# Optimization experiments

Measured on AMD Instinct MI355X. Metric: run time of the kernel, lower is better.

## Reference

```python
import jax, jax.numpy as jnp
import numpy as np

B, T, D, H = 512, 2048, 256, 256  # batch, seq_len, input_size, hidden_size


def _uniform(key, shape, fan_in):
    b = 1.0 / np.sqrt(fan_in)
    return jax.random.uniform(key, shape, minval=-b, maxval=b, dtype=jnp.float32)


def setup_inputs() -> dict:
    key = jax.random.key(0)
    ks = jax.random.split(key, 12)
    return {
        "input_tensor": jax.random.normal(ks[0], (B, T, D), dtype=jnp.float32),
        # fc_i: Linear(D, D)
        "Wi": _uniform(ks[1], (D, D), D), "bi": _uniform(ks[2], (D,), D),
        # fc_h: Linear(H, H)
        "Wh": _uniform(ks[3], (H, H), H), "bh": _uniform(ks[4], (H,), H),
        # fc_a: Linear(D, D)
        "Wa": _uniform(ks[5], (D, D), D), "ba": _uniform(ks[6], (D,), D),
        # LSTM(input_size=D, hidden_size=H), gates ordered [i, f, g, o]
        "W_ih": _uniform(ks[7], (4 * H, D), H), "b_ih": _uniform(ks[8], (4 * H,), H),
        "W_hh": _uniform(ks[9], (4 * H, H), H), "b_hh": _uniform(ks[10], (4 * H,), H),
    }


def reference(input_tensor, Wi, bi, Wh, bh, Wa, ba, W_ih, W_hh, b_ih, b_hh):
    x = input_tensor                      # (B, T, D)
    Bb = x.shape[0]
    Hh = Wh.shape[0]
    h0 = jnp.zeros((Bb, Hh), x.dtype)
    c0 = jnp.zeros((Bb, Hh), x.dtype)

    # Per-timestep FC attention; hidden state never updates in the loop,
    # so it vectorizes exactly over T.
    input_o = jnp.einsum('btd,ed->bte', x, Wi) + bi          # (B, T, D)
    hidden_o = h0 @ Wh.T + bh                                # (B, H) == (B, D)
    pre = input_o + hidden_o[:, None, :]                     # (B, T, D)
    attn = jax.nn.sigmoid(jnp.einsum('btd,ed->bte', pre, Wa) + ba)
    attention_output = jnp.sum(attn * x, axis=1)             # (B, D)

    # LSTM over a length-1 sequence (single cell step), PyTorch gate order i,f,g,o
    gates = attention_output @ W_ih.T + b_ih + h0 @ W_hh.T + b_hh
    i, f, g, o = jnp.split(gates, 4, axis=-1)
    i = jax.nn.sigmoid(i); f = jax.nn.sigmoid(f)
    g = jnp.tanh(g); o = jax.nn.sigmoid(o)
    c = f * c0 + i * g
    h = o * jnp.tanh(c)

    lstm_output = h[None]                                    # (1, B, H)
    return (lstm_output, h[None], c[None])
```

## Files before the change

### kernel.cpp

```cpp
#include <hip/hip_runtime.h>
#include <hip/hip_bf16.h>

typedef _Float16 f16x8 __attribute__((ext_vector_type(8)));
typedef float    f32x4 __attribute__((ext_vector_type(4)));

#define B_SZ 512
#define T_SZ 2048
#define D_SZ 256
#define TCHUNK 64
#define NCHUNK (T_SZ / TCHUNK)

__global__ __launch_bounds__(256) void prep_kernel(
    const float* __restrict__ Wa, const float* __restrict__ Wi,
    const float* __restrict__ bi, const float* __restrict__ bh,
    const float* __restrict__ ba,
    _Float16* __restrict__ Weff, float* __restrict__ beff)
{
    int e = blockIdx.x;
    int d = threadIdx.x;
    float acc = 0.f;
    #pragma unroll 4
    for (int k = 0; k < 256; ++k)
        acc = fmaf(Wa[e*256 + k], Wi[k*256 + d], acc);
    Weff[e*256 + d] = (_Float16)acc;

    __shared__ float red[256];
    red[d] = Wa[e*256 + d] * (bi[d] + bh[d]);
    __syncthreads();
    if (d == 0) {
        float s = ba[e];
        for (int k = 0; k < 256; ++k) s += red[k];
        beff[e] = s;
    }
}

__global__ __launch_bounds__(512) void attn_kernel(
    const float* __restrict__ x,
    const _Float16* __restrict__ Weff,
    const float* __restrict__ beff,
    float* __restrict__ ao)
{
    const int b    = blockIdx.x;
    const int tid  = threadIdx.x;
    const int wave = tid >> 6;
    const int lane = tid & 63;
    const int l15  = lane & 15;
    const int lq   = lane >> 4;

    __shared__ _Float16 xs[TCHUNK * 256];

    f16x8 bfrag[2][8];
    #pragma unroll
    for (int ct = 0; ct < 2; ++ct) {
        int col = wave*32 + ct*16 + l15;
        #pragma unroll
        for (int ks = 0; ks < 8; ++ks) {
            int k0 = ks*32 + lq*8;
            bfrag[ct][ks] = *reinterpret_cast<const f16x8*>(&Weff[col*256 + k0]);
        }
    }
    float bcol[2];
    bcol[0] = beff[wave*32 + l15];
    bcol[1] = beff[wave*32 + 16 + l15];

    const float* xb = x + (size_t)b * T_SZ * D_SZ;

    const int srow = tid >> 5;
    const int scol = (tid & 31) * 8;

    f32x4 regA[4], regB[4];

    {
        const float* src = xb;
        #pragma unroll
        for (int i = 0; i < 4; ++i) {
            const float* p = src + (size_t)(i*16 + srow) * 256 + scol;
            regA[i] = *reinterpret_cast<const f32x4*>(p);
            regB[i] = *reinterpret_cast<const f32x4*>(p + 4);
        }
    }

    float ao_acc0 = 0.f, ao_acc1 = 0.f;

    for (int c = 0; c < NCHUNK; ++c) {
        __syncthreads();
        #pragma unroll
        for (int i = 0; i < 4; ++i) {
            int row = i*16 + srow;
            f16x8 h;
            h[0] = (_Float16)regA[i][0]; h[1] = (_Float16)regA[i][1];
            h[2] = (_Float16)regA[i][2]; h[3] = (_Float16)regA[i][3];
            h[4] = (_Float16)regB[i][0]; h[5] = (_Float16)regB[i][1];
            h[6] = (_Float16)regB[i][2]; h[7] = (_Float16)regB[i][3];
            int byte = (row*512 + scol*2) ^ ((row & 7) << 4);
            *reinterpret_cast<f16x8*>(reinterpret_cast<char*>(xs) + byte) = h;
        }
        __syncthreads();

        if (c + 1 < NCHUNK) {
            const float* src = xb + (size_t)(c + 1) * (TCHUNK * D_SZ);
            #pragma unroll
            for (int i = 0; i < 4; ++i) {
                const float* p = src + (size_t)(i*16 + srow) * 256 + scol;
                regA[i] = *reinterpret_cast<const f32x4*>(p);
                regB[i] = *reinterpret_cast<const f32x4*>(p + 4);
            }
        }

        #pragma unroll
        for (int rt = 0; rt < 4; ++rt) {
            f16x8 afrag[8];
            #pragma unroll
            for (int ks = 0; ks < 8; ++ks) {
                int row = rt*16 + l15;
                int kk  = ks*32 + lq*8;
                int byte = (row*512 + kk*2) ^ ((row & 7) << 4);
                afrag[ks] = *reinterpret_cast<const f16x8*>(
                    reinterpret_cast<const char*>(xs) + byte);
            }
            #pragma unroll
            for (int ct = 0; ct < 2; ++ct) {
                f32x4 acc = {0.f, 0.f, 0.f, 0.f};
                #pragma unroll
                for (int ks = 0; ks < 8; ++ks)
                    acc = __builtin_amdgcn_mfma_f32_16x16x32_f16(
                        afrag[ks], bfrag[ct][ks], acc, 0, 0, 0);
                float bia = bcol[ct];
                int colb = (wave*32 + ct*16 + l15) * 2;
                #pragma unroll
                for (int r = 0; r < 4; ++r) {
                    int row = rt*16 + lq*4 + r;
                    float s = acc[r] + bia;
                    float attn = __builtin_amdgcn_rcpf(1.f + __expf(-s));
                    int byte = (row*512 + colb) ^ ((row & 7) << 4);
                    float xv = (float)*reinterpret_cast<const _Float16*>(
                        reinterpret_cast<const char*>(xs) + byte);
                    if (ct == 0) ao_acc0 = fmaf(attn, xv, ao_acc0);
                    else         ao_acc1 = fmaf(attn, xv, ao_acc1);
                }
            }
        }
    }

    {
        float v = ao_acc0;
        v += __shfl_xor(v, 16, 64);
        v += __shfl_xor(v, 32, 64);
        if (lq == 0) ao[b*256 + wave*32 + l15] = v;
        float w = ao_acc1;
        w += __shfl_xor(w, 16, 64);
        w += __shfl_xor(w, 32, 64);
        if (lq == 0) ao[b*256 + wave*32 + 16 + l15] = w;
    }
}

__global__ __launch_bounds__(256) void lstm_kernel(
    const float* __restrict__ ao,
    const float* __restrict__ Wih,
    const float* __restrict__ bih,
    const float* __restrict__ bhh,
    float* __restrict__ out)
{
    int b = blockIdx.x;
    int j = threadIdx.x;
    __shared__ float a[256];
    a[j] = ao[b*256 + j];
    __syncthreads();

    float gi = bih[j]       + bhh[j];
    float gg = bih[512 + j] + bhh[512 + j];
    float go = bih[768 + j] + bhh[768 + j];
    const float* wi = Wih + (size_t)j * 256;
    const float* wg = Wih + (size_t)(512 + j) * 256;
    const float* wo = Wih + (size_t)(768 + j) * 256;
    #pragma unroll 4
    for (int k = 0; k < 256; k += 4) {
        f32x4 w1 = *reinterpret_cast<const f32x4*>(wi + k);
        f32x4 w2 = *reinterpret_cast<const f32x4*>(wg + k);
        f32x4 w3 = *reinterpret_cast<const f32x4*>(wo + k);
        #pragma unroll
        for (int q = 0; q < 4; ++q) {
            float av = a[k + q];
            gi = fmaf(w1[q], av, gi);
            gg = fmaf(w2[q], av, gg);
            go = fmaf(w3[q], av, go);
        }
    }
    float ig = 1.f / (1.f + __expf(-gi));
    float g  = tanhf(gg);
    float og = 1.f / (1.f + __expf(-go));
    float cc = ig * g;
    float hh = og * tanhf(cc);
    out[          b*256 + j] = hh;
    out[131072 +  b*256 + j] = hh;
    out[262144 +  b*256 + j] = cc;
}

extern "C" void kernel_launch(void* const* d_in, const int* in_sizes, int n_in,
                              void* d_out, int out_size, void* d_ws, size_t ws_size,
                              hipStream_t stream) {
    const float* x    = (const float*)d_in[0];
    const float* Wi   = (const float*)d_in[1];
    const float* bi   = (const float*)d_in[2];
    const float* bh   = (const float*)d_in[4];
    const float* Wa   = (const float*)d_in[5];
    const float* ba   = (const float*)d_in[6];
    const float* W_ih = (const float*)d_in[7];
    const float* b_ih = (const float*)d_in[8];
    const float* b_hh = (const float*)d_in[10];

    char* ws = (char*)d_ws;
    _Float16* Weff = (_Float16*)ws;
    float*    beff = (float*)(ws + 128*1024);
    float*    ao   = (float*)(ws + 132*1024);

    prep_kernel<<<256, 256, 0, stream>>>(Wa, Wi, bi, bh, ba, Weff, beff);
    attn_kernel<<<B_SZ, 512, 0, stream>>>(x, Weff, beff, ao);
    lstm_kernel<<<B_SZ, 256, 0, stream>>>(ao, W_ih, b_ih, b_hh, (float*)d_out);
}
```

Before: 308.8 us.

## Double-buffer x chunks via direct global-to-LDS loads in fp32

The attention kernel now streams x straight into a double-buffered fp32 LDS tile using global_load_lds, in place of loading into registers and converting to fp16 before the shared store. Conversion to fp16 moves to the point where MFMA A-fragments are read. The chunk shrinks to 32 rows so two fp32 buffers fit, and waitcnt/barrier fencing overlaps the next chunk's load with compute. The prep kernel also gets split accumulators and a wave-shuffle bias reduction. This trades more LDS bandwidth and per-fragment conversion work for fewer register staging copies and better load/compute overlap.

After: 420.8 us. 1.36x slower.

```diff
diff --git a/kernel.cpp b/kernel.cpp
--- a/kernel.cpp
+++ b/kernel.cpp
@@ -7,7 +7,7 @@
 #define B_SZ 512
 #define T_SZ 2048
 #define D_SZ 256
-#define TCHUNK 64
+#define TCHUNK 32
 #define NCHUNK (T_SZ / TCHUNK)
 
 __global__ __launch_bounds__(256) void prep_kernel(
@@ -18,23 +18,30 @@
 {
     int e = blockIdx.x;
     int d = threadIdx.x;
-    float acc = 0.f;
+    float a0 = 0.f, a1 = 0.f, a2 = 0.f, a3 = 0.f;
     #pragma unroll 4
-    for (int k = 0; k < 256; ++k)
-        acc = fmaf(Wa[e*256 + k], Wi[k*256 + d], acc);
-    Weff[e*256 + d] = (_Float16)acc;
-
-    __shared__ float red[256];
-    red[d] = Wa[e*256 + d] * (bi[d] + bh[d]);
+    for (int k = 0; k < 256; k += 4) {
+        a0 = fmaf(Wa[e*256 + k    ], Wi[(k    )*256 + d], a0);
+        a1 = fmaf(Wa[e*256 + k + 1], Wi[(k + 1)*256 + d], a1);
+        a2 = fmaf(Wa[e*256 + k + 2], Wi[(k + 2)*256 + d], a2);
+        a3 = fmaf(Wa[e*256 + k + 3], Wi[(k + 3)*256 + d], a3);
+    }
+    Weff[e*256 + d] = (_Float16)((a0 + a1) + (a2 + a3));
+
+    __shared__ float red[4];
+    float s = Wa[e*256 + d] * (bi[d] + bh[d]);
+    s += __shfl_down(s, 32, 64);
+    s += __shfl_down(s, 16, 64);
+    s += __shfl_down(s,  8, 64);
+    s += __shfl_down(s,  4, 64);
+    s += __shfl_down(s,  2, 64);
+    s += __shfl_down(s,  1, 64);
+    if ((d & 63) == 0) red[d >> 6] = s;
     __syncthreads();
-    if (d == 0) {
-        float s = ba[e];
-        for (int k = 0; k < 256; ++k) s += red[k];
-        beff[e] = s;
-    }
-}
-
-__global__ __launch_bounds__(512) void attn_kernel(
+    if (d == 0) beff[e] = ba[e] + ((red[0] + red[1]) + (red[2] + red[3]));
+}
+
+__global__ __launch_bounds__(512, 4) void attn_kernel(
     const float* __restrict__ x,
     const _Float16* __restrict__ Weff,
     const float* __restrict__ beff,
@@ -47,7 +54,7 @@
     const int l15  = lane & 15;
     const int lq   = lane >> 4;
 
-    __shared__ _Float16 xs[TCHUNK * 256];
+    __shared__ float xs[2][TCHUNK * 256];
 
     f16x8 bfrag[2][8];
     #pragma unroll
@@ -59,99 +66,97 @@
             bfrag[ct][ks] = *reinterpret_cast<const f16x8*>(&Weff[col*256 + k0]);
         }
     }
-    float bcol[2];
-    bcol[0] = beff[wave*32 + l15];
-    bcol[1] = beff[wave*32 + 16 + l15];
+    float bcol0 = beff[wave*32 + l15];
+    float bcol1 = beff[wave*32 + 16 + l15];
 
     const float* xb = x + (size_t)b * T_SZ * D_SZ;
 
-    const int srow = tid >> 5;
-    const int scol = (tid & 31) * 8;
-
-    f32x4 regA[4], regB[4];
-
-    {
-        const float* src = xb;
+    #define STAGE(dstbuf, c)                                                          \
+        {                                                                             \
+            _Pragma("unroll")                                                         \
+            for (int i = 0; i < 4; ++i) {                                             \
+                int rw = wave*4 + i;                                                  \
+                int gcol = (lane*16) ^ ((rw & 7) << 4);                               \
+                const char* srcp = (const char*)(xb + (size_t)((c)*TCHUNK + rw)*256) + gcol; \
+                char* dstp = (char*)(&xs[dstbuf][0]) + rw*1024;                       \
+                __builtin_amdgcn_global_load_lds(                                     \
+                    (const __attribute__((address_space(1))) void*)srcp,              \
+                    (__attribute__((address_space(3))) void*)dstp, 16, 0, 0);         \
+            }                                                                         \
+        }
+
+    float ao_acc0 = 0.f, ao_acc1 = 0.f;
+
+    STAGE(0, 0);
+    int cur = 0;
+
+    for (int c = 0; c < NCHUNK; ++c) {
+        if (c + 1 < NCHUNK) {
+            STAGE(cur ^ 1, c + 1);
+            asm volatile("s_waitcnt vmcnt(4)" ::: "memory");
+        } else {
+            asm volatile("s_waitcnt vmcnt(0)" ::: "memory");
+        }
+        __builtin_amdgcn_s_barrier();
+
+        const char* buf = (const char*)(&xs[cur][0]);
+
         #pragma unroll
-        for (int i = 0; i < 4; ++i) {
-            const float* p = src + (size_t)(i*16 + srow) * 256 + scol;
-            regA[i] = *reinterpret_cast<const f32x4*>(p);
-            regB[i] = *reinterpret_cast<const f32x4*>(p + 4);
-        }
-    }
-
-    float ao_acc0 = 0.f, ao_acc1 = 0.f;
-
-    for (int c = 0; c < NCHUNK; ++c) {
-        __syncthreads();
-        #pragma unroll
-        for (int i = 0; i < 4; ++i) {
-            int row = i*16 + srow;
-            f16x8 h;
-            h[0] = (_Float16)regA[i][0]; h[1] = (_Float16)regA[i][1];
-            h[2] = (_Float16)regA[i][2]; h[3] = (_Float16)regA[i][3];
-            h[4] = (_Float16)regB[i][0]; h[5] = (_Float16)regB[i][1];
-            h[6] = (_Float16)regB[i][2]; h[7] = (_Float16)regB[i][3];
-            int byte = (row*512 + scol*2) ^ ((row & 7) << 4);
-            *reinterpret_cast<f16x8*>(reinterpret_cast<char*>(xs) + byte) = h;
-        }
-        __syncthreads();
-
-        if (c + 1 < NCHUNK) {
-            const float* src = xb + (size_t)(c + 1) * (TCHUNK * D_SZ);
-            #pragma unroll
-            for (int i = 0; i < 4; ++i) {
-                const float* p = src + (size_t)(i*16 + srow) * 256 + scol;
-                regA[i] = *reinterpret_cast<const f32x4*>(p);
-                regB[i] = *reinterpret_cast<const f32x4*>(p + 4);
-            }
-        }
-
-        #pragma unroll
-        for (int rt = 0; rt < 4; ++rt) {
-            f16x8 afrag[8];
+        for (int rt = 0; rt < 2; ++rt) {
+            const int arow = rt*16 + l15;
+            const int aswz = (arow & 7) << 4;
+            const int abase = arow*1024;
+            f32x4 acc0 = {0.f, 0.f, 0.f, 0.f};
+            f32x4 acc1 = {0.f, 0.f, 0.f, 0.f};
             #pragma unroll
             for (int ks = 0; ks < 8; ++ks) {
-                int row = rt*16 + l15;
-                int kk  = ks*32 + lq*8;
-                int byte = (row*512 + kk*2) ^ ((row & 7) << 4);
-                afrag[ks] = *reinterpret_cast<const f16x8*>(
-                    reinterpret_cast<const char*>(xs) + byte);
+                int cb0 = ks*128 + lq*32;
+                f32x4 lo = *reinterpret_cast<const f32x4*>(buf + abase + ((cb0     ) ^ aswz));
+                f32x4 hi = *reinterpret_cast<const f32x4*>(buf + abase + ((cb0 + 16) ^ aswz));
+                f16x8 a;
+                a[0] = (_Float16)lo[0]; a[1] = (_Float16)lo[1];
+                a[2] = (_Float16)lo[2]; a[3] = (_Float16)lo[3];
+                a[4] = (_Float16)hi[0]; a[5] = (_Float16)hi[1];
+                a[6] = (_Float16)hi[2]; a[7] = (_Float16)hi[3];
+                acc0 = __builtin_amdgcn_mfma_f32_16x16x32_f16(a, bfrag[0][ks], acc0, 0, 0, 0);
+                acc1 = __builtin_amdgcn_mfma_f32_16x16x32_f16(a, bfrag[1][ks], acc1, 0, 0, 0);
             }
             #pragma unroll
-            for (int ct = 0; ct < 2; ++ct) {
-                f32x4 acc = {0.f, 0.f, 0.f, 0.f};
-                #pragma unroll
-                for (int ks = 0; ks < 8; ++ks)
-                    acc = __builtin_amdgcn_mfma_f32_16x16x32_f16(
-                        afrag[ks], bfrag[ct][ks], acc, 0, 0, 0);
-                float bia = bcol[ct];
-                int colb = (wave*32 + ct*16 + l15) * 2;
-                #pragma unroll
-                for (int r = 0; r < 4; ++r) {
-                    int row = rt*16 + lq*4 + r;
-                    float s = acc[r] + bia;
+            for (int r = 0; r < 4; ++r) {
+                int row  = rt*16 + lq*4 + r;
+                int rswz = (row & 7) << 4;
+                int rb   = row*1024;
+                {
+                    float s = acc0[r] + bcol0;
                     float attn = __builtin_amdgcn_rcpf(1.f + __expf(-s));
-                    int byte = (row*512 + colb) ^ ((row & 7) << 4);
-                    float xv = (float)*reinterpret_cast<const _Float16*>(
-                        reinterpret_cast<const char*>(xs) + byte);
-                    if (ct == 0) ao_acc0 = fmaf(attn, xv, ao_acc0);
-                    else         ao_acc1 = fmaf(attn, xv, ao_acc1);
+                    int cb = ((wave*32 + l15)*4) ^ rswz;
+                    float xv = *reinterpret_cast<const float*>(buf + rb + cb);
+                    ao_acc0 = fmaf(attn, xv, ao_acc0);
+                }
+                {
+                    float s = acc1[r] + bcol1;
+                    float attn = __builtin_amdgcn_rcpf(1.f + __expf(-s));
+                    int cb = ((wave*32 + 16 + l15)*4) ^ rswz;
+                    float xv = *reinterpret_cast<const float*>(buf + rb + cb);
+                    ao_acc1 = fmaf(attn, xv, ao_acc1);
                 }
             }
         }
-    }
-
-    {
-        float v = ao_acc0;
-        v += __shfl_xor(v, 16, 64);
-        v += __shfl_xor(v, 32, 64);
-        if (lq == 0) ao[b*256 + wave*32 + l15] = v;
-        float w = ao_acc1;
-        w += __shfl_xor(w, 16, 64);
-        w += __shfl_xor(w, 32, 64);
-        if (lq == 0) ao[b*256 + wave*32 + 16 + l15] = w;
-    }
+
+        asm volatile("s_waitcnt lgkmcnt(0)" ::: "memory");
+        __builtin_amdgcn_s_barrier();
+        cur ^= 1;
+    }
+
+    float v = ao_acc0;
+    v += __shfl_xor(v, 16, 64);
+    v += __shfl_xor(v, 32, 64);
+    if (lq == 0) ao[b*256 + wave*32 + l15] = v;
+    float w = ao_acc1;
+    w += __shfl_xor(w, 16, 64);
+    w += __shfl_xor(w, 32, 64);
+    if (lq == 0) ao[b*256 + wave*32 + 16 + l15] = w;
+    #undef STAGE
 }
 
 __global__ __launch_bounds__(256) void lstm_kernel(
```
